# Kernel optimization log

Hardware: AMD Instinct MI355X
Metric: run time of the kernel (lower is better)

Reference implementation:

```python
import jax, jax.numpy as jnp
import numpy as np

SEM_DIM = 256
N_LEVELS = 21
HALF = jnp.float32((N_LEVELS - 1) / 2.0)  # 10.0
BETA = 0.1  # commitment cost


def setup_inputs() -> dict:
    key = jax.random.key(0)
    k1, k2 = jax.random.split(key)
    z = jax.random.normal(k1, (8, 292, 2048), dtype=jnp.float32)
    # nn.init.uniform_(codebook.weight, -1/dim, 1/dim)
    codebook = jax.random.uniform(k2, (8192, SEM_DIM), dtype=jnp.float32,
                                  minval=-1.0 / SEM_DIM, maxval=1.0 / SEM_DIM)
    return {"z": z, "codebook": codebook}


def reference(z, codebook):
    # Split latent: semantic (VQ) / acoustic (FSQ)
    z_sem = z[:, :SEM_DIM, :]   # (B, 256, T)
    z_ac = z[:, SEM_DIM:, :]    # (B, 36, T)
    B, D, T = z_sem.shape

    # ---- VectorQuantizer (eval path) ----
    z_flat = jnp.transpose(z_sem, (0, 2, 1)).reshape(B * T, D)  # (BT, D)
    # ||z||^2 - 2 z.c^T + ||c||^2
    dists = (jnp.sum(z_flat * z_flat, axis=1, keepdims=True)
             - 2.0 * jnp.einsum('nd,kd->nk', z_flat, codebook)
             + jnp.sum(codebook * codebook, axis=1)[None, :])  # (BT, K)
    indices = jnp.argmin(dists, axis=1)  # (BT,)
    z_q = codebook[indices].reshape(B, T, D).transpose(0, 2, 1)  # (B, D, T)

    codebook_loss = jnp.mean((z_q - jax.lax.stop_gradient(z_sem)) ** 2)
    commitment_loss = BETA * jnp.mean((jax.lax.stop_gradient(z_q) - z_sem) ** 2)
    vq_loss = codebook_loss + commitment_loss

    # straight-through
    z_sem_q = z_sem + jax.lax.stop_gradient(z_q - z_sem)

    # ---- FSQ quantize (eval path) ----
    z_b = jnp.tanh(z_ac) * HALF
    z_ac_q = z_b + jax.lax.stop_gradient(jnp.round(z_b) - z_b)  # round STE
    ac_codes = jnp.clip(jnp.round(z_ac_q + HALF).astype(jnp.int32), 0, N_LEVELS - 1)

    z_out = jnp.concatenate([z_sem_q, z_ac_q], axis=1)  # (B, 292, T)
    return z_out, indices.reshape(B, T), ac_codes, vq_loss, z_ac_q
```

## Files before the change

kernel.cpp:

```cpp
#include <hip/hip_runtime.h>
#include <cfloat>
#include <math.h>

#define BQ 8
#define T 2048
#define D 256
#define DAC 36
#define CH 292
#define K 8192
#define NROWS (BQ*T)
#define TAU 1e-3f
#define FSPLIT 4
#define RSPLIT 16
#define CAPROWS 8192

#define OFF_IDX   (BQ*CH*T)
#define OFF_CODES (OFF_IDX + NROWS)
#define OFF_LOSS  (OFF_CODES + BQ*DAC*T)
#define OFF_ACQ   (OFF_LOSS + 1)

#define WN_C2    0
#define WN_Z2    32768
#define WN_CNT   98304
#define WN_LIST  98560
#define WN_LOSS  164096
#define WN_WIDX  168192
#define WN_PMX   262144
#define WN_PR    262144
#define WN_AZ    2359296
#define WN_ZG    2359296
#define WN_BC    10747904
#define WN_NEED  14942208

#define WS_C2    0
#define WS_Z2    32768
#define WS_PART  131072
#define WS_IDX   655360
#define WS_LOSS  720896
#define MT 32
#define KT 128
#define DC 32
#define NSPLIT 4

typedef float f32x4 __attribute__((ext_vector_type(4)));
typedef __bf16 bf16x8 __attribute__((ext_vector_type(8)));
typedef __attribute__((address_space(1))) const unsigned int gu32;
typedef __attribute__((address_space(3))) unsigned int lu32;

__device__ inline void gl_lds16(const void* gp, void* lp) {
    __builtin_amdgcn_global_load_lds((gu32*)gp, (lu32*)lp, 16, 0, 0);
}

__device__ inline unsigned short f2bf(float x) {
    unsigned u = __float_as_uint(x);
    return (unsigned short)((u + 0x7fffu + ((u >> 16) & 1u)) >> 16);
}

__device__ inline void merge3(float& m1, float& m2, int& mi, float o1, float o2, int oi) {
    if (o1 < m1 || (o1 == m1 && oi < mi)) { m2 = fminf(m1, o2); m1 = o1; mi = oi; }
    else                                  { m2 = fminf(m2, o1); }
}

template <typename F>
__device__ float np_pairwise256_sq(F ld) {
    float S[2];
    #pragma unroll
    for (int h = 0; h < 2; h++) {
        int base = h * 128;
        float v[16];
        #pragma unroll
        for (int l = 0; l < 16; l++) {
            float q[8];
            #pragma unroll
            for (int j = 0; j < 8; j++) { float x = ld(base + j * 16 + l); q[j] = x * x; }
            v[l] = ((q[0] + q[1]) + (q[2] + q[3])) + ((q[4] + q[5]) + (q[6] + q[7]));
        }
        float t1[8], t2[4], t3[2];
        #pragma unroll
        for (int l = 0; l < 8; l++) t1[l] = v[l] + v[l + 8];
        #pragma unroll
        for (int l = 0; l < 4; l++) t2[l] = t1[l] + t1[l + 4];
        t3[0] = t2[0] + t2[2]; t3[1] = t2[1] + t2[3];
        S[h] = t3[0] + t3[1];
    }
    return S[0] + S[1];
}

__global__ void k_c2pw(const float* __restrict__ cb, float* __restrict__ c2) {
    int k = blockIdx.x * 256 + threadIdx.x;
    const float* row = cb + (size_t)k * D;
    c2[k] = np_pairwise256_sq([&](int d) { return row[d]; });
}

__global__ void k_z2pw(const float* __restrict__ z, float* __restrict__ z2) {
    int n = blockIdx.x * 256 + threadIdx.x;
    int b = n >> 11, t = n & 2047;
    const float* base = z + (size_t)b * CH * T + t;
    z2[n] = np_pairwise256_sq([&](int d) { return base[(size_t)d * T]; });
}

__global__ __launch_bounds__(256) void k_prep(const float* __restrict__ z,
        const float* __restrict__ cb, unsigned short* __restrict__ Az,
        unsigned short* __restrict__ Bc, float* __restrict__ c2,
        float* __restrict__ z2, int* __restrict__ cnt, float* __restrict__ out) {
    __shared__ float zt[32][260];
    const int tid = threadIdx.x;
    if ((int)blockIdx.x < (K / 4)) {
        const int w = tid >> 6, l = tid & 63;
        const int k = blockIdx.x * 4 + w;
        float4 v = *(const float4*)(cb + (size_t)k * D + l * 4);
        *(float4*)&zt[w][l * 4] = v;
        float fa[4] = {v.x, v.y, v.z, v.w};
        unsigned short hh[4];
        #pragma unroll
        for (int e = 0; e < 4; e++) hh[e] = f2bf(fa[e]);
        *(uint2*)(Bc + (size_t)k * 256 + l * 4) = *(uint2*)hh;
        __syncthreads();
        if (tid < 4) {
            int kk = blockIdx.x * 4 + tid;
            c2[kk] = np_pairwise256_sq([&](int d) { return zt[tid][d]; });
        }
        if (blockIdx.x == 0 && tid == 0) *cnt = 0;
    } else if ((int)blockIdx.x < (K / 4) + 512) {
        const int bb = blockIdx.x - (K / 4);
        const int b = bb >> 6, t0 = (bb & 63) * 32;
        for (int i = tid; i < 2048; i += 256) {
            int d = i >> 3, tq = (i & 7) * 4;
            float4 v = *(const float4*)(z + (size_t)(b * CH + d) * T + t0 + tq);
            zt[tq + 0][d] = v.x; zt[tq + 1][d] = v.y;
            zt[tq + 2][d] = v.z; zt[tq + 3][d] = v.w;
        }
        __syncthreads();
        const int t = tid >> 3, c8 = tid & 7;
        unsigned short* rowp = Az + (size_t)(b * 2048 + t0 + t) * 256;
        #pragma unroll
        for (int li = 0; li < 4; li++) {
            int u = c8 + 8 * li;
            int dbase = u * 8;
            float f[8];
            *(float4*)&f[0] = *(float4*)&zt[t][dbase];
            *(float4*)&f[4] = *(float4*)&zt[t][dbase + 4];
            unsigned short h[8];
            #pragma unroll
            for (int e = 0; e < 8; e++) h[e] = f2bf(f[e]);
            *(uint4*)(rowp + u * 8) = *(uint4*)h;
        }
        if (tid < 32)
            z2[b * 2048 + t0 + tid] = np_pairwise256_sq([&](int d) { return zt[tid][d]; });
    } else {
        const int ab = blockIdx.x - ((K / 4) + 512);
        int i = (ab * 256 + tid) * 4;
        int b = i / (DAC * T);
        int r = i % (DAC * T);
        int d = r / T, t = r % T;
        size_t zoff = ((size_t)(b * CH + 256 + d)) * T + t;
        float4 v = *(const float4*)(z + zoff);
        float r0, r1, r2, r3;
        {
            float t0 = (float)tanh((double)v.x); r0 = rintf(t0 * 10.0f);
            float t1 = (float)tanh((double)v.y); r1 = rintf(t1 * 10.0f);
            float t2 = (float)tanh((double)v.z); r2 = rintf(t2 * 10.0f);
            float t3 = (float)tanh((double)v.w); r3 = rintf(t3 * 10.0f);
        }
        *(float4*)(out + zoff) = make_float4(r0, r1, r2, r3);
        size_t co = OFF_CODES + (size_t)(b * DAC + d) * T + t;
        *(float4*)(out + co) = make_float4(r0 + 10.0f, r1 + 10.0f, r2 + 10.0f, r3 + 10.0f);
        size_t ao = OFF_ACQ + (size_t)(b * DAC + d) * T + t;
        out[ao + 0] = r0; out[ao + 1] = r1; out[ao + 2] = r2; out[ao + 3] = r3;
    }
}

__global__ __launch_bounds__(256, 2) void k_fast(
        const unsigned short* __restrict__ Az, const unsigned short* __restrict__ Bc,
        const float* __restrict__ c2g, float4* __restrict__ pmx) {
    __shared__ __align__(16) unsigned char smem8[65536];
    __shared__ float c2s[2048];

    const int tid = threadIdx.x;
    const int w = tid >> 6, lane = tid & 63;
    const int quad = lane >> 4, c = lane & 15;

    const int sp = blockIdx.x >> 7;
    const int nt = blockIdx.x & 127;
    const int n0 = nt * 128;
    const int kbase = sp * 2048;

    const char* Azb = (const char*)Az;
    const char* Bcb = (const char*)Bc;

    #pragma unroll
    for (int i = 0; i < 8; i++) c2s[tid + i * 256] = c2g[kbase + tid + i * 256];

    const int hi2 = lane >> 5;
    const char* sq[8];
    #pragma unroll
    for (int q = 0; q < 8; q++) {
        const int seg = w * 8 + q;
        const int code = seg * 2 + hi2;
        sq[q] = Bcb + (size_t)(kbase + code) * 512 + (((lane & 31) ^ (code & 7)) << 4);
    }
    auto stage = [&](int t, int buf) {
        unsigned char* base = smem8 + buf * 32768;
        #pragma unroll
        for (int q = 0; q < 8; q++)
            gl_lds16(sq[q] + (size_t)t * 32768, base + (w * 8 + q) * 1024);
    };

    int voff[8];
    #pragma unroll
    for (int ks = 0; ks < 8; ks++)
        voff[ks] = c * 512 + (((((ks << 2) | quad) ^ (c & 7))) << 4);

    bf16x8 af[2][8];
    #pragma unroll
    for (int i = 0; i < 2; i++)
        #pragma unroll
        for (int ks = 0; ks < 8; ks++)
            af[i][ks] = *(const bf16x8*)(Azb +
                (size_t)(n0 + w * 32 + i * 16 + c) * 512 + ks * 64 + quad * 16);

    float bm1[8], bm2[8]; int bid[8];
    #pragma unroll
    for (int sl = 0; sl < 8; sl++) { bm1[sl] = FLT_MAX; bm2[sl] = FLT_MAX; bid[sl] = 0x7fffffff; }

    f32x4 accA[2][4], accB[2][4];

    #define MFMA_TILE(BUFC, ACC) do {                                         \
        _Pragma("unroll")                                                     \
        for (int i = 0; i < 2; i++)                                           \
            _Pragma("unroll")                                                 \
            for (int j = 0; j < 4; j++) ACC[i][j] = (f32x4)0.0f;              \
        __builtin_amdgcn_s_setprio(1);                                        \
        _Pragma("unroll")                                                     \
        for (int j = 0; j < 4; j++) {                                         \
            bf16x8 bf[8];                                                     \
            _Pragma("unroll")                                                 \
            for (int ks = 0; ks < 8; ks++)                                    \
                bf[ks] = *(const bf16x8*)(smem8 + voff[ks] +                  \
                                          ((BUFC) * 32768 + j * 8192));       \
            _Pragma("unroll")                                                 \
            for (int ks = 0; ks < 8; ks++) {                 \
                ACC[0][j] = __builtin_amdgcn_mfma_f32_16x16x32_bf16(af[0][ks], bf[ks], ACC[0][j], 0, 0, 0); \
                ACC[1][j] = __builtin_amdgcn_mfma_f32_16x16x32_bf16(af[1][ks], bf[ks], ACC[1][j], 0, 0, 0); \
            }                                                                 \
        }                                                                     \
        __builtin_amdgcn_s_setprio(0);                                        \
    } while (0)

    auto epilogue = [&](int t, f32x4 (&acc)[2][4]) {
        const int k0 = kbase + t * 64;
        #pragma unroll
        for (int j = 0; j < 4; j++) {
            const int kk = k0 + j * 16 + c;
            const float c2v = c2s[t * 64 + j * 16 + c];
            #pragma unroll
            for (int i = 0; i < 2; i++)
                #pragma unroll
                for (int r = 0; r < 4; r++) {
                    float sc = fmaf(-2.0f, acc[i][j][r], c2v);
                    int sl = i * 4 + r;
                    bm2[sl] = __builtin_amdgcn_fmed3f(bm1[sl], sc, bm2[sl]);
                    if (sc < bm1[sl]) { bm1[sl] = sc; bid[sl] = kk; }
                }
        }
    };

    stage(0, 0);
    __syncthreads();
    stage(1, 1);
    MFMA_TILE(0, accA);

    #define FITER(T, BUF, CUR, PRV) do {                                  \
        asm volatile("s_waitcnt vmcnt(0)" ::: "memory");                  \
        __builtin_amdgcn_s_barrier();                                     \
        __builtin_amdgcn_sched_barrier(0);                                \
        if ((T) < 31) stage((T) + 1, (BUF) ^ 1);                          \
        MFMA_TILE(BUF, CUR);                                              \
        epilogue((T) - 1, PRV);                                           \
    } while (0)

    for (int tt = 1; tt < 31; tt += 2) {
        FITER(tt,     1, accB, accA);
        FITER(tt + 1, 0, accA, accB);
    }
    FITER(31, 1, accB, accA);
    epilogue(31, accB);
    #undef FITER
    #undef MFMA_TILE

    #pragma unroll
    for (int mask = 1; mask <= 8; mask <<= 1)
        #pragma unroll
        for (int sl = 0; sl < 8; sl++) {
            float o1 = __shfl_xor(bm1[sl], mask, 64);
            float o2 = __shfl_xor(bm2[sl], mask, 64);
            int   oi = __shfl_xor(bid[sl], mask, 64);
            merge3(bm1[sl], bm2[sl], bid[sl], o1, o2, oi);
        }
    if (c == 0) {
        #pragma unroll
        for (int i = 0; i < 2; i++)
            #pragma unroll
            for (int r = 0; r < 4; r++) {
                int row = w * 32 + i * 16 + quad * 4 + r, sl = i * 4 + r;
                pmx[(size_t)sp * NROWS + n0 + row] =
                    make_float4(bm1[sl], bm2[sl], __int_as_float(bid[sl]), 0.f);
            }
    }
}

__global__ __launch_bounds__(256) void k_reduce2(const float4* __restrict__ pmx,
                          int* __restrict__ widx,
                          int* __restrict__ cnt, int* __restrict__ list,
                          float* __restrict__ out, const float* __restrict__ z,
                          float* __restrict__ zg) {
    __shared__ int lrow[256], lpos[256];
    __shared__ int lcnt;
    const int tid = threadIdx.x;
    if (tid == 0) lcnt = 0;
    __syncthreads();
    int n = blockIdx.x * 256 + tid;
    float a1 = FLT_MAX, a2 = FLT_MAX; int ai = 0x7fffffff;
    #pragma unroll
    for (int s = 0; s < FSPLIT; s++) {
        float4 p = pmx[(size_t)s * NROWS + n];
        merge3(a1, a2, ai, p.x, p.y, __float_as_int(p.z));
    }
    if (a2 - a1 < TAU) {
        int pos = atomicAdd(cnt, 1);
        list[pos] = n;
        widx[n] = ~pos;
        int l = atomicAdd(&lcnt, 1);
        lrow[l] = n; lpos[l] = pos;
    } else {
        widx[n] = ai;
        out[OFF_IDX + n] = (float)ai;
    }
    __syncthreads();
    const int lc = lcnt;
    for (int it = 0; it < lc; it++) {
        int pos = lpos[it];
        if (pos < CAPROWS) {
            int rn = lrow[it];
            zg[(size_t)pos * D + tid] =
                z[((size_t)((rn >> 11) * CH + tid)) * T + (rn & 2047)];
        }
    }
}

__global__ __launch_bounds__(256, 2) void k_rescuex(
        const float* __restrict__ z, const float* __restrict__ cb,
        const float* __restrict__ c2, const float* __restrict__ z2,
        const int* __restrict__ cnt, const int* __restrict__ list,
        const float* __restrict__ zg, float2* __restrict__ pr) {
    __shared__ float zs[D][MT + 4];
    __shared__ float cs[2][DC][KT + 4];
    __shared__ float c2s[K / RSPLIT];
    __shared__ int   ls[MT];
    __shared__ float z2sh[MT];
    const int tid = threadIdx.x;
    const int tx = tid & 31, ty = tid >> 5;
    const int grp = blockIdx.x >> 4, sp = blockIdx.x & 15;
    const int cntv = *cnt;
    const int base = grp * MT;
    if (base >= cntv) return;
    const int nr = min(MT, cntv - base);
    const int kbase = sp * (K / RSPLIT);
    const int kl = tid & 127, half = tid >> 7;

    if (tid < MT) {
        int pos = base + ((tid < nr) ? tid : (nr - 1));
        int n = list[pos];
        ls[tid] = n;
        z2sh[tid] = z2[n];
    }
    #pragma unroll
    for (int i = 0; i < (K / RSPLIT) / 256; i++)
        c2s[tid + i * 256] = c2[kbase + tid + i * 256];

    float4 rv0, rv1, rv2, rv3;
    auto ldchunk = [&](int ch) {
        const int k0 = kbase + (ch >> 3) * KT, dcc = (ch & 7) * DC;
        const float4* src = (const float4*)(cb + (size_t)(k0 + kl) * D + dcc + half * 16);
        rv0 = src[0]; rv1 = src[1]; rv2 = src[2]; rv3 = src[3];
    };
    auto wrchunk = [&](int b) {
        const int dl = half * 16;
        cs[b][dl + 0][kl] = rv0.x; cs[b][dl + 1][kl] = rv0.y;
        cs[b][dl + 2][kl] = rv0.z; cs[b][dl + 3][kl] = rv0.w;
        cs[b][dl + 4][kl] = rv1.x; cs[b][dl + 5][kl] = rv1.y;
        cs[b][dl + 6][kl] = rv1.z; cs[b][dl + 7][kl] = rv1.w;
        cs[b][dl + 8][kl] = rv2.x; cs[b][dl + 9][kl] = rv2.y;
        cs[b][dl + 10][kl] = rv2.z; cs[b][dl + 11][kl] = rv2.w;
        cs[b][dl + 12][kl] = rv3.x; cs[b][dl + 13][kl] = rv3.y;
        cs[b][dl + 14][kl] = rv3.z; cs[b][dl + 15][kl] = rv3.w;
    };

    if (base + MT <= CAPROWS) {
        ldchunk(0);
        for (int i = tid; i < MT * 64; i += 256) {
            int r = i >> 6, dq = (i & 63) << 2;
            float4 v = *(const float4*)(zg + (size_t)(base + r) * D + dq);
            zs[dq + 0][r] = v.x; zs[dq + 1][r] = v.y;
            zs[dq + 2][r] = v.z; zs[dq + 3][r] = v.w;
        }
    } else {
        __syncthreads();
        for (int i = tid; i < D * MT; i += 256) {
            int d = i >> 5, r = i & 31;
            int n = ls[r];
            zs[d][r] = z[((size_t)((n >> 11) * CH + d)) * T + (n & 2047)];
        }
        ldchunk(0);
    }
    __syncthreads();
    wrchunk(0);
    ldchunk(1);
    asm volatile("s_waitcnt lgkmcnt(0)" ::: "memory");
    __builtin_amdgcn_s_barrier();
    __builtin_amdgcn_sched_barrier(0);

    float z2r[4];
    #pragma unroll
    for (int i = 0; i < 4; i++) z2r[i] = z2sh[ty * 4 + i];

    float m1[4]; int bi[4];
    #pragma unroll
    for (int i = 0; i < 4; i++) { m1[i] = FLT_MAX; bi[i] = 0x7fffffff; }
    float acc[4][4] = {};

    const int NCH = (K / RSPLIT) / KT * (D / DC);
    for (int ch = 0; ch < NCH; ch++) {
        const int b = ch & 1;
        const int dcc = (ch & 7) * DC;
        #pragma unroll 8
        for (int d = 0; d < DC; d++) {
            const float4 zf = *(const float4*)&zs[dcc + d][ty * 4];
            const float4 cf = *(const float4*)&cs[b][d][tx * 4];
            const float za[4] = {zf.x, zf.y, zf.z, zf.w};
            const float ca[4] = {cf.x, cf.y, cf.z, cf.w};
            #pragma unroll
            for (int i = 0; i < 4; i++)
                #pragma unroll
                for (int j = 0; j < 4; j++)
                    acc[i][j] = fmaf(za[i], ca[j], acc[i][j]);
        }
        if ((ch & 7) == 7) {
            const int koff = (ch >> 3) * KT;
            #pragma unroll
            for (int j = 0; j < 4; j++) {
                int kk = kbase + koff + tx * 4 + j;
                float c2v = c2s[koff + tx * 4 + j];
                #pragma unroll
                for (int i = 0; i < 4; i++) {
                    float tpre = z2r[i] - 2.0f * acc[i][j];
                    float s = tpre + c2v;
                    if (s < m1[i]) { m1[i] = s; bi[i] = kk; }
                }
            }
            #pragma unroll
            for (int i = 0; i < 4; i++)
                #pragma unroll
                for (int j = 0; j < 4; j++) acc[i][j] = 0.0f;
        }
        if (ch < NCH - 1) {
            __syncthreads();
            wrchunk(b ^ 1);
            if (ch < NCH - 2) ldchunk(ch + 2);
            asm volatile("s_waitcnt lgkmcnt(0)" ::: "memory");
            __builtin_amdgcn_s_barrier();
            __builtin_amdgcn_sched_barrier(0);
        }
    }
    __syncthreads();
    float* rm1 = (float*)zs;
    int*   rix = (int*)(rm1 + MT * 32);
    #pragma unroll
    for (int i = 0; i < 4; i++) {
        int slot = (ty * 4 + i) * 32 + tx;
        rm1[slot] = m1[i]; rix[slot] = bi[i];
    }
    __syncthreads();
    if (tid < MT) {
        float a1 = FLT_MAX; int ai = 0x7fffffff;
        for (int t = 0; t < 32; t++) {
            float b1 = rm1[tid * 32 + t]; int bidx = rix[tid * 32 + t];
            if (b1 < a1 || (b1 == a1 && bidx < ai)) { a1 = b1; ai = bidx; }
        }
        if (tid < nr)
            pr[(size_t)sp * NROWS + base + tid] = make_float2(a1, __int_as_float(ai));
    }
}

__global__ __launch_bounds__(256) void k_exact(
        const float* __restrict__ z, const float* __restrict__ cb,
        const float* __restrict__ c2, const float* __restrict__ z2,
        float2* __restrict__ part) {
    __shared__ float zs[D][MT];
    __shared__ float cs[DC][KT + 4];
    const int tid = threadIdx.x;
    const int tx = tid & 31, ty = tid >> 5;
    const int n0 = blockIdx.x * MT;
    const int bb = n0 >> 11, t0 = n0 & 2047;
    const int kbase = blockIdx.y * (K / NSPLIT);
    for (int i = tid; i < D * (MT / 4); i += 256) {
        int d = i >> 3, tg = i & 7;
        float4 v = *(const float4*)(z + ((size_t)(bb * CH + d)) * T + t0 + tg * 4);
        *(float4*)&zs[d][tg * 4] = v;
    }
    float z2r[4];
    #pragma unroll
    for (int i = 0; i < 4; i++) z2r[i] = z2[n0 + ty * 4 + i];
    float m1[4]; int bi[4];
    #pragma unroll
    for (int i = 0; i < 4; i++) { m1[i] = FLT_MAX; bi[i] = 0x7fffffff; }
    for (int ktt = 0; ktt < K / NSPLIT; ktt += KT) {
        const int k0 = kbase + ktt;
        float acc[4][4] = {};
        for (int dc = 0; dc < D; dc += DC) {
            __syncthreads();
            {
                int kl = tid & 127, half = tid >> 7;
                const float4* src = (const float4*)(cb + (size_t)(k0 + kl) * D + dc + half * 16);
                #pragma unroll
                for (int j = 0; j < 4; j++) {
                    float4 v = src[j];
                    int dl = half * 16 + j * 4;
                    cs[dl + 0][kl] = v.x; cs[dl + 1][kl] = v.y;
                    cs[dl + 2][kl] = v.z; cs[dl + 3][kl] = v.w;
                }
            }
            __syncthreads();
            #pragma unroll 8
            for (int d = 0; d < DC; d++) {
                const float4 zf = *(const float4*)&zs[dc + d][ty * 4];
                const float4 cf = *(const float4*)&cs[d][tx * 4];
                const float za[4] = {zf.x, zf.y, zf.z, zf.w};
                const float ca[4] = {cf.x, cf.y, cf.z, cf.w};
                #pragma unroll
                for (int i = 0; i < 4; i++)
                    #pragma unroll
                    for (int j = 0; j < 4; j++)
                        acc[i][j] = fmaf(za[i], ca[j], acc[i][j]);
            }
        }
        #pragma unroll
        for (int j = 0; j < 4; j++) {
            int kk = k0 + tx * 4 + j;
            float c2v = c2[kk];
            #pragma unroll
            for (int i = 0; i < 4; i++) {
                float tpre = z2r[i] - 2.0f * acc[i][j];
                float s = tpre + c2v;
                if (s < m1[i]) { m1[i] = s; bi[i] = kk; }
            }
        }
    }
    __syncthreads();
    float* rm1 = (float*)zs;
    int*   rix = (int*)(rm1 + MT * 32);
    #pragma unroll
    for (int i = 0; i < 4; i++) {
        int slot = (ty * 4 + i) * 32 + tx;
        rm1[slot] = m1[i]; rix[slot] = bi[i];
    }
    __syncthreads();
    if (tid < MT) {
        float a1 = FLT_MAX; int ai = 0x7fffffff;
        for (int t = 0; t < 32; t++) {
            float b1 = rm1[tid * 32 + t]; int bidx = rix[tid * 32 + t];
            if (b1 < a1 || (b1 == a1 && bidx < ai)) { a1 = b1; ai = bidx; }
        }
        part[(size_t)(n0 + tid) * NSPLIT + blockIdx.y] = make_float2(a1, __int_as_float(ai));
    }
}

__global__ void k_reduce(const float2* __restrict__ part, int* __restrict__ widx,
                         float* __restrict__ out) {
    int n = blockIdx.x * 256 + threadIdx.x;
    float a1 = FLT_MAX; int ai = 0x7fffffff;
    #pragma unroll
    for (int s = 0; s < NSPLIT; s++) {
        float2 p = part[(size_t)n * NSPLIT + s];
        float b1 = p.x; int bidx = __float_as_int(p.y);
        if (b1 < a1 || (b1 == a1 && bidx < ai)) { a1 = b1; ai = bidx; }
    }
    widx[n] = ai;
    out[OFF_IDX + n] = (float)ai;
}

__global__ __launch_bounds__(256) void k_episem(
        const float* __restrict__ z, const float* __restrict__ cb,
        const int* __restrict__ widx, const float2* __restrict__ pr,
        float* __restrict__ out, double* __restrict__ lossp) {
    __shared__ int qidx[32];
    __shared__ float qs[32][260];
    __shared__ double wsum[4];
    const int tid = threadIdx.x;
    const int bb = blockIdx.x >> 6;
    const int t0 = (blockIdx.x & 63) * 32;
    if (tid < 32) {
        int n = bb * T + t0 + tid;
        int wv = widx[n];
        if (wv < 0) {
            int pos = ~wv;
            float a1 = FLT_MAX; int ai = 0x7fffffff;
            #pragma unroll
            for (int s = 0; s < RSPLIT; s++) {
                float2 p = pr[(size_t)s * NROWS + pos];
                float v = p.x; int ix = __float_as_int(p.y);
                if (v < a1 || (v == a1 && ix < ai)) { a1 = v; ai = ix; }
            }
            wv = ai;
            out[OFF_IDX + n] = (float)ai;
        }
        qidx[tid] = wv;
    }
    __syncthreads();
    for (int i = tid; i < 32 * 64; i += 256) {
        int tl = i >> 6, lanee = i & 63;
        float4 v = *(const float4*)(cb + (size_t)qidx[tl] * D + lanee * 4);
        *(float4*)&qs[tl][lanee * 4] = v;
    }
    __syncthreads();
    double ls = 0.0;
    for (int it = 0; it < 32; it++) {
        int d = it * 8 + (tid >> 5);
        int tl = tid & 31;
        size_t ga = ((size_t)(bb * CH + d)) * T + t0 + tl;
        float q = qs[tl][d];
        float e = q - z[ga];
        out[ga] = q;
        ls += (double)e * (double)e;
    }
    #pragma unroll
    for (int off = 32; off; off >>= 1) ls += __shfl_down(ls, off, 64);
    if ((tid & 63) == 0) wsum[tid >> 6] = ls;
    __syncthreads();
    if (tid == 0) lossp[blockIdx.x] = wsum[0] + wsum[1] + wsum[2] + wsum[3];
}

__global__ void k_loss(const double* __restrict__ lossp, float* __restrict__ out) {
    __shared__ double sm[256];
    int tid = threadIdx.x;
    sm[tid] = lossp[tid] + lossp[tid + 256];
    __syncthreads();
    for (int off = 128; off; off >>= 1) {
        if (tid < off) sm[tid] += sm[tid + off];
        __syncthreads();
    }
    if (tid == 0) out[OFF_LOSS] = (float)(1.1 * sm[0] / (double)(BQ * D * T));
}

__global__ __launch_bounds__(256) void k_episemf(
        const float* __restrict__ z, const float* __restrict__ cb,
        const int* __restrict__ widx, float* __restrict__ out, double* __restrict__ lossp) {
    __shared__ int qidx[32];
    __shared__ float qs[32][260];
    __shared__ double wsum[4];
    const int tid = threadIdx.x;
    const int bb = blockIdx.x >> 6;
    const int t0 = (blockIdx.x & 63) * 32;
    if (tid < 32) qidx[tid] = widx[bb * T + t0 + tid];
    __syncthreads();
    for (int i = tid; i < 32 * 64; i += 256) {
        int tl = i >> 6, lanee = i & 63;
        float4 v = *(const float4*)(cb + (size_t)qidx[tl] * D + lanee * 4);
        *(float4*)&qs[tl][lanee * 4] = v;
    }
    __syncthreads();
    double ls = 0.0;
    for (int it = 0; it < 32; it++) {
        int d = it * 8 + (tid >> 5);
        int tl = tid & 31;
        size_t ga = ((size_t)(bb * CH + d)) * T + t0 + tl;
        float q = qs[tl][d];
        float e = q - z[ga];
        out[ga] = q;
        ls += (double)e * (double)e;
    }
    #pragma unroll
    for (int off = 32; off; off >>= 1) ls += __shfl_down(ls, off, 64);
    if ((tid & 63) == 0) wsum[tid >> 6] = ls;
    __syncthreads();
    if (tid == 0) lossp[blockIdx.x] = wsum[0] + wsum[1] + wsum[2] + wsum[3];
}

__global__ void k_epiac(const float* __restrict__ z, const double* __restrict__ lossp,
                        float* __restrict__ out) {
    __shared__ double sm[256];
    int i = (blockIdx.x * 256 + threadIdx.x) * 4;
    int b = i / (DAC * T);
    int r = i % (DAC * T);
    int d = r / T, t = r % T;
    size_t zoff = ((size_t)(b * CH + 256 + d)) * T + t;
    float4 v = *(const float4*)(z + zoff);
    float r0, r1, r2, r3;
    {
        float t0 = (float)tanh((double)v.x); r0 = rintf(t0 * 10.0f);
        float t1 = (float)tanh((double)v.y); r1 = rintf(t1 * 10.0f);
        float t2 = (float)tanh((double)v.z); r2 = rintf(t2 * 10.0f);
        float t3 = (float)tanh((double)v.w); r3 = rintf(t3 * 10.0f);
    }
    *(float4*)(out + zoff) = make_float4(r0, r1, r2, r3);
    size_t co = OFF_CODES + (size_t)(b * DAC + d) * T + t;
    *(float4*)(out + co) = make_float4(r0 + 10.0f, r1 + 10.0f, r2 + 10.0f, r3 + 10.0f);
    size_t ao = OFF_ACQ + (size_t)(b * DAC + d) * T + t;
    out[ao + 0] = r0; out[ao + 1] = r1; out[ao + 2] = r2; out[ao + 3] = r3;
    if (blockIdx.x == 0) {
        int tid = threadIdx.x;
        sm[tid] = lossp[tid] + lossp[tid + 256];
        __syncthreads();
        for (int off = 128; off; off >>= 1) {
            if (tid < off) sm[tid] += sm[tid + off];
            __syncthreads();
        }
        if (tid == 0) out[OFF_LOSS] = (float)(1.1 * sm[0] / (double)(BQ * D * T));
    }
}

extern "C" void kernel_launch(void* const* d_in, const int* in_sizes, int n_in,
                              void* d_out, int out_size, void* d_ws, size_t ws_size,
                              hipStream_t stream) {
    const float* z  = (const float*)d_in[0];
    const float* cb = (const float*)d_in[1];
    float* out = (float*)d_out;
    char* ws = (char*)d_ws;

    if (ws_size >= (size_t)WN_NEED) {
        float*  c2    = (float*)(ws + WN_C2);
        float*  z2    = (float*)(ws + WN_Z2);
        int*    cnt   = (int*)(ws + WN_CNT);
        int*    list  = (int*)(ws + WN_LIST);
        double* lossp = (double*)(ws + WN_LOSS);
        int*    widx  = (int*)(ws + WN_WIDX);
        float4* pmx   = (float4*)(ws + WN_PMX);
        unsigned short* Az = (unsigned short*)(ws + WN_AZ);
        unsigned short* Bc = (unsigned short*)(ws + WN_BC);
        float*  zg    = (float*)(ws + WN_ZG);
        float2* pr    = (float2*)(ws + WN_PR);

        hipLaunchKernelGGL(k_prep,    dim3(K / 4 + 512 + BQ * DAC * T / 1024), dim3(256), 0, stream,
                           z, cb, Az, Bc, c2, z2, cnt, out);
        hipLaunchKernelGGL(k_fast,    dim3(128 * FSPLIT), dim3(256), 0, stream, Az, Bc, c2, pmx);
        hipLaunchKernelGGL(k_reduce2, dim3(NROWS / 256),  dim3(256), 0, stream,
                           pmx, widx, cnt, list, out, z, zg);
        hipLaunchKernelGGL(k_rescuex, dim3((NROWS / MT) * RSPLIT), dim3(256), 0, stream,
                           z, cb, c2, z2, cnt, list, zg, pr);
        hipLaunchKernelGGL(k_episem,  dim3(BQ * (T / 32)), dim3(256), 0, stream,
                           z, cb, widx, pr, out, lossp);
        hipLaunchKernelGGL(k_loss,    dim3(1),            dim3(256), 0, stream, lossp, out);
    } else {
        float*  c2    = (float*)(ws + WS_C2);
        float*  z2    = (float*)(ws + WS_Z2);
        float2* part  = (float2*)(ws + WS_PART);
        int*    widx  = (int*)(ws + WS_IDX);
        double* lossp = (double*)(ws + WS_LOSS);
        hipLaunchKernelGGL(k_c2pw,   dim3(K / 256),            dim3(256), 0, stream, cb, c2);
        hipLaunchKernelGGL(k_z2pw,   dim3(NROWS / 256),        dim3(256), 0, stream, z, z2);
        hipLaunchKernelGGL(k_exact,  dim3(NROWS / MT, NSPLIT), dim3(256), 0, stream, z, cb, c2, z2, part);
        hipLaunchKernelGGL(k_reduce, dim3(NROWS / 256),        dim3(256), 0, stream, part, widx, out);
        hipLaunchKernelGGL(k_episemf, dim3(BQ * (T / 32)),     dim3(256), 0, stream, z, cb, widx, out, lossp);
        hipLaunchKernelGGL(k_epiac,  dim3(BQ * DAC * T / 1024), dim3(256), 0, stream, z, lossp, out);
    }
}
```

Before: 269.0 us.

## Rescue only codebook splits whose fast-pass minimum is within tolerance

For ambiguous rows, k_reduce2 records which of the four fast-pass codebook splits had a candidate within TAU of the best, and queues the row into a per-split list. The exact fp32 rescue kernel then handles each codebook quarter only for rows queued on it, instead of all 8192 codes for every ambiguous row. The epilogue merges only the flagged partial results, decoded from a bitmask packed into widx. This cuts rescue FLOPs and codebook traffic, at the cost of extra atomics, an indirect row lookup, and a dependence on the fast pass's per-split minima being accurate to within TAU.

Result: faster. 255.0 us, median of 2 (-5.2%).

```diff
diff --git a/kernel.cpp b/kernel.cpp
--- a/kernel.cpp
+++ b/kernel.cpp
@@ -25,12 +25,14 @@
 #define WN_LIST  98560
 #define WN_LOSS  164096
 #define WN_WIDX  168192
+#define WN_QCNT  233728
 #define WN_PMX   262144
 #define WN_PR    262144
 #define WN_AZ    2359296
 #define WN_ZG    2359296
 #define WN_BC    10747904
-#define WN_NEED  14942208
+#define WN_QL    14942208
+#define WN_NEED  15204352
 
 #define WS_C2    0
 #define WS_Z2    32768
@@ -102,7 +104,8 @@
 __global__ __launch_bounds__(256) void k_prep(const float* __restrict__ z,
         const float* __restrict__ cb, unsigned short* __restrict__ Az,
         unsigned short* __restrict__ Bc, float* __restrict__ c2,
-        float* __restrict__ z2, int* __restrict__ cnt, float* __restrict__ out) {
+        float* __restrict__ z2, int* __restrict__ cnt, int* __restrict__ qcnt,
+        float* __restrict__ out) {
     __shared__ float zt[32][260];
     const int tid = threadIdx.x;
     if ((int)blockIdx.x < (K / 4)) {
@@ -120,7 +123,10 @@
             int kk = blockIdx.x * 4 + tid;
             c2[kk] = np_pairwise256_sq([&](int d) { return zt[tid][d]; });
         }
-        if (blockIdx.x == 0 && tid == 0) *cnt = 0;
+        if (blockIdx.x == 0) {
+            if (tid == 0) *cnt = 0;
+            if (tid < 4) qcnt[tid] = 0;
+        }
     } else if ((int)blockIdx.x < (K / 4) + 512) {
         const int bb = blockIdx.x - (K / 4);
         const int b = bb >> 6, t0 = (bb & 63) * 32;
@@ -313,23 +319,34 @@
                           int* __restrict__ widx,
                           int* __restrict__ cnt, int* __restrict__ list,
                           float* __restrict__ out, const float* __restrict__ z,
-                          float* __restrict__ zg) {
+                          float* __restrict__ zg, int* __restrict__ qcnt,
+                          int* __restrict__ ql) {
     __shared__ int lrow[256], lpos[256];
     __shared__ int lcnt;
     const int tid = threadIdx.x;
     if (tid == 0) lcnt = 0;
     __syncthreads();
     int n = blockIdx.x * 256 + tid;
+    float4 pv[FSPLIT];
     float a1 = FLT_MAX, a2 = FLT_MAX; int ai = 0x7fffffff;
     #pragma unroll
     for (int s = 0; s < FSPLIT; s++) {
-        float4 p = pmx[(size_t)s * NROWS + n];
-        merge3(a1, a2, ai, p.x, p.y, __float_as_int(p.z));
+        pv[s] = pmx[(size_t)s * NROWS + n];
+        merge3(a1, a2, ai, pv[s].x, pv[s].y, __float_as_int(pv[s].z));
     }
     if (a2 - a1 < TAU) {
         int pos = atomicAdd(cnt, 1);
         list[pos] = n;
-        widx[n] = ~pos;
+        int mask = 0;
+        #pragma unroll
+        for (int s = 0; s < FSPLIT; s++) {
+            if (pv[s].x <= a1 + TAU) {
+                mask |= 1 << s;
+                int qp = atomicAdd(&qcnt[s], 1);
+                ql[s * NROWS + qp] = pos;
+            }
+        }
+        widx[n] = ~(pos | (mask << 14));
         int l = atomicAdd(&lcnt, 1);
         lrow[l] = n; lpos[l] = pos;
     } else {
@@ -351,31 +368,36 @@
 __global__ __launch_bounds__(256, 2) void k_rescuex(
         const float* __restrict__ z, const float* __restrict__ cb,
         const float* __restrict__ c2, const float* __restrict__ z2,
-        const int* __restrict__ cnt, const int* __restrict__ list,
+        const int* __restrict__ list, const int* __restrict__ qcnt,
+        const int* __restrict__ ql,
         const float* __restrict__ zg, float2* __restrict__ pr) {
     __shared__ float zs[D][MT + 4];
     __shared__ float cs[2][DC][KT + 4];
-    __shared__ float c2s[K / RSPLIT];
+    __shared__ float c2s[512];
     __shared__ int   ls[MT];
+    __shared__ int   lpo[MT];
     __shared__ float z2sh[MT];
     const int tid = threadIdx.x;
     const int tx = tid & 31, ty = tid >> 5;
-    const int grp = blockIdx.x >> 4, sp = blockIdx.x & 15;
-    const int cntv = *cnt;
+    const int fs = blockIdx.x & 3, sub = (blockIdx.x >> 2) & 3;
+    const int grp = blockIdx.x >> 4;
+    const int qc = qcnt[fs];
     const int base = grp * MT;
-    if (base >= cntv) return;
-    const int nr = min(MT, cntv - base);
-    const int kbase = sp * (K / RSPLIT);
+    if (base >= qc) return;
+    const int nr = min(MT, qc - base);
+    const int kbase = fs * 2048 + sub * 512;
+    const int rs = fs * 4 + sub;
     const int kl = tid & 127, half = tid >> 7;
 
     if (tid < MT) {
-        int pos = base + ((tid < nr) ? tid : (nr - 1));
+        int qi = base + ((tid < nr) ? tid : (nr - 1));
+        int pos = ql[fs * NROWS + qi];
         int n = list[pos];
-        ls[tid] = n;
+        ls[tid] = n; lpo[tid] = pos;
         z2sh[tid] = z2[n];
     }
     #pragma unroll
-    for (int i = 0; i < (K / RSPLIT) / 256; i++)
+    for (int i = 0; i < 2; i++)
         c2s[tid + i * 256] = c2[kbase + tid + i * 256];
 
     float4 rv0, rv1, rv2, rv3;
@@ -396,22 +418,21 @@
         cs[b][dl + 14][kl] = rv3.z; cs[b][dl + 15][kl] = rv3.w;
     };
 
-    if (base + MT <= CAPROWS) {
-        ldchunk(0);
-        for (int i = tid; i < MT * 64; i += 256) {
-            int r = i >> 6, dq = (i & 63) << 2;
-            float4 v = *(const float4*)(zg + (size_t)(base + r) * D + dq);
+    ldchunk(0);
+    __syncthreads();
+    for (int i = tid; i < MT * 64; i += 256) {
+        int r = i >> 6, dq = (i & 63) << 2;
+        int po = lpo[r];
+        if (po < CAPROWS) {
+            float4 v = *(const float4*)(zg + (size_t)po * D + dq);
             zs[dq + 0][r] = v.x; zs[dq + 1][r] = v.y;
             zs[dq + 2][r] = v.z; zs[dq + 3][r] = v.w;
-        }
-    } else {
-        __syncthreads();
-        for (int i = tid; i < D * MT; i += 256) {
-            int d = i >> 5, r = i & 31;
+        } else {
             int n = ls[r];
-            zs[d][r] = z[((size_t)((n >> 11) * CH + d)) * T + (n & 2047)];
-        }
-        ldchunk(0);
+            #pragma unroll
+            for (int e = 0; e < 4; e++)
+                zs[dq + e][r] = z[((size_t)((n >> 11) * CH + dq + e)) * T + (n & 2047)];
+        }
     }
     __syncthreads();
     wrchunk(0);
@@ -429,7 +450,7 @@
     for (int i = 0; i < 4; i++) { m1[i] = FLT_MAX; bi[i] = 0x7fffffff; }
     float acc[4][4] = {};
 
-    const int NCH = (K / RSPLIT) / KT * (D / DC);
+    const int NCH = (512 / KT) * (D / DC);
     for (int ch = 0; ch < NCH; ch++) {
         const int b = ch & 1;
         const int dcc = (ch & 7) * DC;
@@ -488,7 +509,7 @@
             if (b1 < a1 || (b1 == a1 && bidx < ai)) { a1 = b1; ai = bidx; }
         }
         if (tid < nr)
-            pr[(size_t)sp * NROWS + base + tid] = make_float2(a1, __int_as_float(ai));
+            pr[(size_t)rs * NROWS + lpo[tid]] = make_float2(a1, __int_as_float(ai));
     }
 }
 
@@ -603,13 +624,17 @@
         int n = bb * T + t0 + tid;
         int wv = widx[n];
         if (wv < 0) {
-            int pos = ~wv;
+            unsigned u = ~wv;
+            int pos = u & 16383;
+            int mask = (u >> 14) & 15;
             float a1 = FLT_MAX; int ai = 0x7fffffff;
             #pragma unroll
             for (int s = 0; s < RSPLIT; s++) {
-                float2 p = pr[(size_t)s * NROWS + pos];
-                float v = p.x; int ix = __float_as_int(p.y);
-                if (v < a1 || (v == a1 && ix < ai)) { a1 = v; ai = ix; }
+                if ((mask >> (s >> 2)) & 1) {
+                    float2 p = pr[(size_t)s * NROWS + pos];
+                    float v = p.x; int ix = __float_as_int(p.y);
+                    if (v < a1 || (v == a1 && ix < ai)) { a1 = v; ai = ix; }
+                }
             }
             wv = ai;
             out[OFF_IDX + n] = (float)ai;
@@ -734,6 +759,8 @@
         int*    list  = (int*)(ws + WN_LIST);
         double* lossp = (double*)(ws + WN_LOSS);
         int*    widx  = (int*)(ws + WN_WIDX);
+        int*    qcnt  = (int*)(ws + WN_QCNT);
+        int*    ql    = (int*)(ws + WN_QL);
         float4* pmx   = (float4*)(ws + WN_PMX);
         unsigned short* Az = (unsigned short*)(ws + WN_AZ);
         unsigned short* Bc = (unsigned short*)(ws + WN_BC);
@@ -741,12 +768,12 @@
         float2* pr    = (float2*)(ws + WN_PR);
 
         hipLaunchKernelGGL(k_prep,    dim3(K / 4 + 512 + BQ * DAC * T / 1024), dim3(256), 0, stream,
-                           z, cb, Az, Bc, c2, z2, cnt, out);
+                           z, cb, Az, Bc, c2, z2, cnt, qcnt, out);
         hipLaunchKernelGGL(k_fast,    dim3(128 * FSPLIT), dim3(256), 0, stream, Az, Bc, c2, pmx);
         hipLaunchKernelGGL(k_reduce2, dim3(NROWS / 256),  dim3(256), 0, stream,
-                           pmx, widx, cnt, list, out, z, zg);
+                           pmx, widx, cnt, list, out, z, zg, qcnt, ql);
         hipLaunchKernelGGL(k_rescuex, dim3((NROWS / MT) * RSPLIT), dim3(256), 0, stream,
-                           z, cb, c2, z2, cnt, list, zg, pr);
+                           z, cb, c2, z2, list, qcnt, ql, zg, pr);
         hipLaunchKernelGGL(k_episem,  dim3(BQ * (T / 32)), dim3(256), 0, stream,
                            z, cb, widx, pr, out, lossp);
         hipLaunchKernelGGL(k_loss,    dim3(1),            dim3(256), 0, stream, lossp, out);
```
